# Kernel tuning notes

Hardware: AMD Instinct MI355X
Metric: run time of the kernel (lower is better)

## Reference

```python
import jax, jax.numpy as jnp
import numpy as np
import math

B, S, H = 8, 1024, 768
NH = 12
DH = H // NH


def _linear(x, W, b):
    # torch Linear: y = x @ W.T + b, W: [out, in]
    return jnp.einsum('bsd,ed->bse', x, W) + b


def _split_heads(x):
    # [B,S,H] -> [B,NH,S,DH]
    b, s, _ = x.shape
    return x.reshape(b, s, NH, DH).transpose(0, 2, 1, 3)


def _attend(q, k, v):
    # q,k,v: [B,NH,S,DH]
    scores = jnp.einsum('bhqd,bhkd->bhqk', q, k) / math.sqrt(DH)
    probs = jax.nn.softmax(scores, axis=-1)
    ctx = jnp.einsum('bhqk,bhkd->bhqd', probs, v)
    b, h, s, d = ctx.shape
    return ctx.transpose(0, 2, 1, 3).reshape(b, s, h * d)


def setup_inputs() -> dict:
    key = jax.random.key(0)
    ks = jax.random.split(key, 20)
    sc = 1.0 / math.sqrt(H)
    inp = {
        'hidden_statesx': jax.random.normal(ks[0], (B, S, H), jnp.float32),
        'hidden_statesy': jax.random.normal(ks[1], (B, S, H), jnp.float32),
    }
    names = ['Wq', 'Wk', 'Wv', 'Wo', 'Wqd', 'Wkd', 'Wvd', 'Wod']
    for i, n in enumerate(names):
        inp[n] = jax.random.normal(ks[2 + i], (H, H), jnp.float32) * sc
        inp['b' + n[1:]] = jnp.zeros((H,), jnp.float32)
    inp['w11'] = jnp.full((1,), 0.5, jnp.float32)
    inp['w12'] = jnp.full((1,), 0.5, jnp.float32)
    inp['w21'] = jnp.full((1,), 0.5, jnp.float32)
    inp['w22'] = jnp.full((1,), 0.5, jnp.float32)
    return inp


def reference(hidden_statesx, hidden_statesy,
              Wq, bq, Wk, bk, Wv, bv, Wo, bo,
              Wqd, bqd, Wkd, bkd, Wvd, bvd, Wod, bod,
              w11, w12, w21, w22):
    q = _split_heads(_linear(hidden_statesx, Wq, bq))
    k = _split_heads(_linear(hidden_statesx, Wk, bk))
    v = _split_heads(_linear(hidden_statesx, Wv, bv))
    qd = _split_heads(_linear(hidden_statesy, Wqd, bqd))
    kd = _split_heads(_linear(hidden_statesy, Wkd, bkd))
    vd = _split_heads(_linear(hidden_statesy, Wvd, bvd))

    # self-attention on x and y streams
    attention_sx = _linear(_attend(q, k, v), Wo, bo)
    attention_sy = _linear(_attend(qd, kd, vd), Wod, bod)
    # cross attentions (mba mode)
    attention_cx = _linear(_attend(q, kd, vd), Wo, bo)
    attention_cy = _linear(_attend(qd, k, v), Wod, bod)

    attention_sx = w11 * attention_sx + w12 * attention_cx
    attention_sy = w21 * attention_sy + w22 * attention_cy
    return attention_sx, attention_sy
```

## Files before the change

kernel.cpp:

```cpp
#include <hip/hip_runtime.h>

typedef __bf16 bf16;
typedef __bf16 bf16x8 __attribute__((ext_vector_type(8)));
typedef float f32x4 __attribute__((ext_vector_type(4)));

#define HD 768
#define ELTS 6291456
#define WELTS 589824

__device__ __forceinline__ void gld_lds16(const bf16* g, bf16* l) {
  __builtin_amdgcn_global_load_lds((const __attribute__((address_space(1))) void*)g,
                                   (__attribute__((address_space(3))) void*)l, 16, 0, 0);
}

__device__ __forceinline__ float rdscalar(const void* p, int f) {
  return f ? (float)((const bf16*)p)[0] : ((const float*)p)[0];
}

__device__ __forceinline__ float exp2fast(float x) {
#if __has_builtin(__builtin_amdgcn_exp2f)
  return __builtin_amdgcn_exp2f(x);
#else
  return __builtin_exp2f(x);
#endif
}

__global__ void probe_dtype(const unsigned int* __restrict__ x, int* flag) {
  const int t = threadIdx.x;
  int bad = 0;
#pragma unroll
  for (int i = 0; i < 4; ++i) {
    unsigned int wd = x[t * 4 + i];
    unsigned int e0 = (wd >> 7) & 0xFF;
    unsigned int e1 = (wd >> 23) & 0xFF;
    bad += (e0 >= 134) + (e1 >= 134);
  }
  unsigned long long m = __ballot(bad > 0);
  if (t == 0) *flag = (m == 0ULL) ? 1 : 0;
}

struct CvtArgs {
  const float* src[20];
  bf16* dst[20];
  int n[20];
  const int* flag;
};
__global__ __launch_bounds__(256) void convert_inputs(CvtArgs a) {
  if (*a.flag) return;
  const int seg = blockIdx.y;
  const float* s = a.src[seg];
  bf16* d = a.dst[seg];
  const int n4 = a.n[seg] >> 2;
  for (int i = blockIdx.x * blockDim.x + threadIdx.x; i < n4; i += gridDim.x * blockDim.x) {
    f32x4 v = *(const f32x4*)(s + i * 4);
    bf16 o[4];
#pragma unroll
    for (int e = 0; e < 4; ++e) o[e] = (bf16)v[e];
    *(unsigned long long*)(d + i * 4) = *(unsigned long long*)o;
  }
}

struct GemmArgs {
  const void* A[6];
  const void* Ac[6];
  const void* W[6];
  const void* Wc[6];
  const void* bias[6];
  const void* biasc[6];
  const void* s0[6];
  const void* s1[6];
  void* C[6];
  float cmul[6];
  int c_fixed[6];
  int vt[6];
  int ext_w[6];
  long long out_elem_off[6];
  const int* flag;
};

__global__ __launch_bounds__(256) void gemm_bt(GemmArgs args) {
  const int g = blockIdx.z;
  const int f = *args.flag;
  const bool c_bf = args.c_fixed[g] || f;
  const bool w_f32 = (!f) && args.ext_w[g];
  const bf16* __restrict__ A = (const bf16*)(f ? args.A[g] : args.Ac[g]);
  const void* __restrict__ Wp = f ? args.W[g] : args.Wc[g];
  const void* __restrict__ bias = f ? args.bias[g] : args.biasc[g];
  bf16* Cb = (bf16*)args.C[g] + args.out_elem_off[g];
  float* Cf = (float*)args.C[g] + args.out_elem_off[g];
  float bscale = 1.0f;
  if (args.s0[g]) bscale = rdscalar(args.s0[g], f) + rdscalar(args.s1[g], f);
  const float cmul = args.cmul[g];

  const int m0 = blockIdx.x * 128;
  const int n0 = blockIdx.y * 128;
  const int t = threadIdx.x;
  const int lane = t & 63;
  const int w = t >> 6;
  const int wm = (w >> 1) * 64, wn = (w & 1) * 64;

  __shared__ __attribute__((aligned(16))) bf16 As[128 * 64];
  __shared__ __attribute__((aligned(16))) bf16 Bs[128 * 64];

  f32x4 acc[4][4] = {};

  const int row_s = t >> 3, slot_s = t & 7;
  const int gswz = (slot_s ^ (row_s & 7)) << 3;

  const int fr = lane & 15;
  const int l4 = lane >> 4;
  const int sR0 = ((l4) ^ (fr & 7)) << 3;
  const int sR1 = ((4 + l4) ^ (fr & 7)) << 3;

  for (int kb = 0; kb < 12; ++kb) {
    const int k0 = kb * 64;
#pragma unroll
    for (int i = 0; i < 4; ++i) {
      const int row = row_s + i * 32;
      gld_lds16(A + (size_t)(m0 + row) * HD + k0 + gswz, As + (t + i * 256) * 8);
    }
    if (!w_f32) {
#pragma unroll
      for (int i = 0; i < 4; ++i) {
        const int row = row_s + i * 32;
        gld_lds16((const bf16*)Wp + (size_t)(n0 + row) * HD + k0 + gswz, Bs + (t + i * 256) * 8);
      }
    } else {
      const float* Wf = (const float*)Wp;
#pragma unroll
      for (int i = 0; i < 4; ++i) {
        const int row = row_s + i * 32;
        const size_t src = (size_t)(n0 + row) * HD + k0 + gswz;
        f32x4 u0 = *(const f32x4*)(Wf + src), u1 = *(const f32x4*)(Wf + src + 4);
        bf16x8 v;
#pragma unroll
        for (int e = 0; e < 4; ++e) { v[e] = (bf16)u0[e]; v[e + 4] = (bf16)u1[e]; }
        *(bf16x8*)(Bs + (t + i * 256) * 8) = v;
      }
    }
    __syncthreads();
#pragma unroll
    for (int kk = 0; kk < 2; ++kk) {
      const int sR = kk ? sR1 : sR0;
      bf16x8 af[4], bfr[4];
#pragma unroll
      for (int mi = 0; mi < 4; ++mi)
        af[mi] = *(const bf16x8*)(As + (wm + mi * 16 + fr) * 64 + sR);
#pragma unroll
      for (int ni = 0; ni < 4; ++ni)
        bfr[ni] = *(const bf16x8*)(Bs + (wn + ni * 16 + fr) * 64 + sR);
#pragma unroll
      for (int mi = 0; mi < 4; ++mi)
#pragma unroll
        for (int ni = 0; ni < 4; ++ni)
          acc[mi][ni] = __builtin_amdgcn_mfma_f32_16x16x32_bf16(af[mi], bfr[ni], acc[mi][ni], 0, 0, 0);
    }
    __syncthreads();
  }

  const int rq = (lane >> 4) * 4;
  const int is_vt = args.vt[g];
#pragma unroll
  for (int ni = 0; ni < 4; ++ni) {
    const int col = n0 + wn + ni * 16 + fr;
    const float bv = (w_f32 ? ((const float*)bias)[col]
                            : (float)((const bf16*)bias)[col]) * bscale;
#pragma unroll
    for (int mi = 0; mi < 4; ++mi) {
      const int row = m0 + wm + mi * 16 + rq;
      if (is_vt) {
        const int bb = row >> 10, s = row & 1023;
        const int hh = col >> 6, d = col & 63;
        bf16 tmp[4];
#pragma unroll
        for (int r = 0; r < 4; ++r) tmp[r] = (bf16)((acc[mi][ni][r] + bv) * cmul);
        *(unsigned long long*)(Cb + (((size_t)(bb * 12 + hh)) << 16) + (d << 10) + s) =
            *(const unsigned long long*)tmp;
      } else {
#pragma unroll
        for (int r = 0; r < 4; ++r) {
          const float val = (acc[mi][ni][r] + bv) * cmul;
          if (c_bf) Cb[(size_t)(row + r) * HD + col] = (bf16)val;
          else      Cf[(size_t)(row + r) * HD + col] = val;
        }
      }
    }
  }
}

__global__ __launch_bounds__(256, 4) void attn_mba(
    const bf16* __restrict__ Q, const bf16* __restrict__ Kx, const bf16* __restrict__ Vtx,
    const bf16* __restrict__ Qd, const bf16* __restrict__ Kd, const bf16* __restrict__ Vtd,
    const void* w11, const void* w12, const void* w21, const void* w22,
    bf16* ctxX, bf16* ctxY, const int* flag) {
  const int linear = blockIdx.x + (blockIdx.y << 4);
  const int swz = (linear & 7) * 192 + (linear >> 3);
  const int qb = swz & 15;
  const int bh = swz >> 4;
  const int b = bh / 12;
  const int f = *flag;

  const float wgtX[2] = {rdscalar(w11, f), rdscalar(w12, f)};
  const float wgtY[2] = {rdscalar(w22, f), rdscalar(w21, f)};

  const size_t tok0 = (size_t)b * 1024;
  const size_t vbase = (size_t)bh * 65536;
  const int fcol = (bh - b * 12) * 64;
  const int q0 = qb * 64;

  __shared__ __attribute__((aligned(16))) bf16 smem[16384];
  bf16* Ks = smem;
  bf16* Vs = smem + 8192;

  const int t = threadIdx.x, lane = t & 63, w = t >> 6;
  const int l15 = lane & 15, l4 = lane >> 4;

  auto stage = [&](int nit) {
    const bf16* Kc = nit < 16 ? Kx : Kd;
    const bf16* Vc = nit < 16 ? Vtx : Vtd;
    const int kt = nit & 15;
    bf16* Kb = Ks + (nit & 1) * 4096;
    bf16* Vb = Vs + (nit & 1) * 4096;
#pragma unroll
    for (int i = 0; i < 2; ++i) {
      const int q = t + i * 256;
      const int g = q >> 3, slot = q & 7;
      const int gs = (slot ^ (g & 7)) << 3;
      const int kp = (g & 32) + ((g & 12) << 1) + ((g & 16) >> 2) + (g & 3);
      gld_lds16(Kc + (tok0 + kt * 64 + kp) * HD + fcol + gs, Kb + q * 8);
      gld_lds16(Vc + vbase + (size_t)g * 1024 + kt * 64 + gs, Vb + q * 8);
    }
  };

  stage(0);

  const int qrow = w * 16 + l15;
  const bf16* qb0 = Q  + (tok0 + q0 + qrow) * HD + fcol;
  const bf16* qb1 = Qd + (tok0 + q0 + qrow) * HD + fcol;
  bf16x8 qf[2][2];
  qf[0][0] = *(const bf16x8*)(qb0 + (l4 << 3));
  qf[0][1] = *(const bf16x8*)(qb0 + ((4 + l4) << 3));
  qf[1][0] = *(const bf16x8*)(qb1 + (l4 << 3));
  qf[1][1] = *(const bf16x8*)(qb1 + ((4 + l4) << 3));

  int koff0[4], koff1[4];
#pragma unroll
  for (int mi = 0; mi < 4; ++mi) {
    const int kr = mi * 16 + l15;
    koff0[mi] = kr * 64 + ((l4 ^ (kr & 7)) << 3);
    koff1[mi] = kr * 64 + (((4 + l4) ^ (kr & 7)) << 3);
  }

  __syncthreads();

  f32x4 mixX[4] = {}, mixY[4] = {};
  f32x4 oacc[2][4] = {};
  float m_s[2] = {-INFINITY, -INFINITY};
  float l_s[2] = {0.0f, 0.0f};

  for (int it = 0; it < 32; ++it) {
    if (it) __syncthreads();
    if (it + 1 < 32) stage(it + 1);
    const bf16* Kb = Ks + (it & 1) * 4096;
    const bf16* Vb = Vs + (it & 1) * 4096;

#pragma unroll
    for (int s2 = 0; s2 < 2; ++s2) {
      float pv[4][4];
      float mx = -INFINITY;
      __builtin_amdgcn_s_setprio(1);
#pragma unroll
      for (int mi = 0; mi < 4; ++mi) {
        bf16x8 kf0 = *(const bf16x8*)(Kb + koff0[mi]);
        bf16x8 kf1 = *(const bf16x8*)(Kb + koff1[mi]);
        f32x4 s = {};
        s = __builtin_amdgcn_mfma_f32_16x16x32_bf16(kf0, qf[s2][0], s, 0, 0, 0);
        s = __builtin_amdgcn_mfma_f32_16x16x32_bf16(kf1, qf[s2][1], s, 0, 0, 0);
        pv[mi][0] = s[0]; pv[mi][1] = s[1]; pv[mi][2] = s[2]; pv[mi][3] = s[3];
        mx = fmaxf(fmaxf(mx, s[0]), s[1]);
        mx = fmaxf(fmaxf(mx, s[2]), s[3]);
      }
      __builtin_amdgcn_s_setprio(0);
      mx = fmaxf(mx, __shfl_xor(mx, 16));
      mx = fmaxf(mx, __shfl_xor(mx, 32));

      if (!__all(mx <= m_s[s2] + 8.0f)) {
        const float mnew = fmaxf(m_s[s2], mx);
        const float alpha = exp2fast(m_s[s2] - mnew);
        l_s[s2] *= alpha;
#pragma unroll
        for (int mi = 0; mi < 4; ++mi) oacc[s2][mi] *= alpha;
        m_s[s2] = mnew;
      }

      float sum = 0.0f;
#pragma unroll
      for (int mi = 0; mi < 4; ++mi)
#pragma unroll
        for (int r = 0; r < 4; ++r) {
          pv[mi][r] = exp2fast(pv[mi][r] - m_s[s2]);
          sum += pv[mi][r];
        }
      sum += __shfl_xor(sum, 16);
      sum += __shfl_xor(sum, 32);
      l_s[s2] += sum;

#pragma unroll
      for (int c = 0; c < 2; ++c) {
        bf16x8 pf;
#pragma unroll
        for (int j = 0; j < 8; ++j)
          pf[j] = (bf16)pv[2 * c + (j >> 2)][j & 3];
        __builtin_amdgcn_s_setprio(1);
#pragma unroll
        for (int mi = 0; mi < 4; ++mi) {
          bf16x8 vf = *(const bf16x8*)(Vb + (c ? koff1[mi] : koff0[mi]));
          oacc[s2][mi] = __builtin_amdgcn_mfma_f32_16x16x32_bf16(vf, pf, oacc[s2][mi], 0, 0, 0);
        }
        __builtin_amdgcn_s_setprio(0);
      }
    }

    if ((it & 15) == 15) {
      const int ph = it >> 4;
      const float scX = wgtX[ph] / l_s[0];
      const float scY = wgtY[ph] / l_s[1];
#pragma unroll
      for (int mi = 0; mi < 4; ++mi) {
#pragma unroll
        for (int r = 0; r < 4; ++r) {
          mixX[mi][r] += scX * oacc[0][mi][r];
          mixY[mi][r] += scY * oacc[1][mi][r];
        }
        oacc[0][mi] = f32x4{};
        oacc[1][mi] = f32x4{};
      }
      m_s[0] = m_s[1] = -INFINITY;
      l_s[0] = l_s[1] = 0.0f;
    }
  }

  __syncthreads();
  bf16* TX = smem;
  bf16* TY = smem + 4608;
#pragma unroll
  for (int mi = 0; mi < 4; ++mi)
#pragma unroll
    for (int r = 0; r < 4; ++r) {
      TX[qrow * 72 + mi * 16 + l4 * 4 + r] = (bf16)mixX[mi][r];
      TY[qrow * 72 + mi * 16 + l4 * 4 + r] = (bf16)mixY[mi][r];
    }
  __syncthreads();
#pragma unroll
  for (int i = 0; i < 2; ++i) {
    const int q = t + i * 256;
    const int g = q >> 3, dc = (q & 7) * 8;
    *(bf16x8*)(ctxX + (tok0 + q0 + g) * HD + fcol + dc) = *(const bf16x8*)(TX + g * 72 + dc);
    *(bf16x8*)(ctxY + (tok0 + q0 + g) * HD + fcol + dc) = *(const bf16x8*)(TY + g * 72 + dc);
  }
}

extern "C" void kernel_launch(void* const* d_in, const int* in_sizes, int n_in,
                              void* d_out, int out_size, void* d_ws, size_t ws_size,
                              hipStream_t stream) {
  (void)in_sizes; (void)n_in; (void)out_size;
  const void* x = d_in[0];
  const void* y = d_in[1];

  bf16* ws = (bf16*)d_ws;
  bf16* Qb   = ws + 0ull * ELTS;
  bf16* Kb   = ws + 1ull * ELTS;
  bf16* Vtb  = ws + 2ull * ELTS;
  bf16* Qdb  = ws + 3ull * ELTS;
  bf16* Kdb  = ws + 4ull * ELTS;
  bf16* Vtdb = ws + 5ull * ELTS;
  bf16* ctxX = Qb;
  bf16* ctxY = Qdb;
  int* flag = (int*)(ws + 6ull * ELTS);

  const size_t extra_elems = 6ull * ELTS + 32 + 2ull * WELTS + 2 * 768;
  const bool big_ws = ws_size >= extra_elems * sizeof(bf16);
  bf16* extraW = ws + 6ull * ELTS + 32;
  bf16* extraB = extraW + 2ull * WELTS;

  bf16* cb = (bf16*)d_out;
  bf16* xb = cb;
  bf16* yb = cb + (size_t)ELTS;
  bf16* Wcv = cb + 2ull * ELTS;
  bf16* bcv = Wcv + 6ull * WELTS;

  probe_dtype<<<dim3(1), dim3(64), 0, stream>>>((const unsigned int*)x, flag);

  CvtArgs ca;
  int nseg = 14;
  {
    const int wsrc[6] = {2, 4, 6, 10, 12, 14};
    ca.src[0] = (const float*)x;  ca.dst[0] = xb;  ca.n[0] = ELTS;
    ca.src[1] = (const float*)y;  ca.dst[1] = yb;  ca.n[1] = ELTS;
    for (int i = 0; i < 6; ++i) {
      ca.src[2 + i] = (const float*)d_in[wsrc[i]];
      ca.dst[2 + i] = Wcv + (size_t)i * WELTS;
      ca.n[2 + i] = WELTS;
      ca.src[8 + i] = (const float*)d_in[wsrc[i] + 1];
      ca.dst[8 + i] = bcv + (size_t)i * 768;
      ca.n[8 + i] = 768;
    }
    if (big_ws) {
      ca.src[14] = (const float*)d_in[8];  ca.dst[14] = extraW;         ca.n[14] = WELTS;
      ca.src[15] = (const float*)d_in[16]; ca.dst[15] = extraW + WELTS; ca.n[15] = WELTS;
      ca.src[16] = (const float*)d_in[9];  ca.dst[16] = extraB;         ca.n[16] = 768;
      ca.src[17] = (const float*)d_in[17]; ca.dst[17] = extraB + 768;   ca.n[17] = 768;
      nseg = 18;
    }
    ca.flag = flag;
  }
  convert_inputs<<<dim3(512, nseg), dim3(256), 0, stream>>>(ca);

  GemmArgs gq;
  {
    const void* A6[6]  = {x, x, x, y, y, y};
    const void* Ac6[6] = {xb, xb, xb, yb, yb, yb};
    const int di[6] = {2, 4, 6, 10, 12, 14};
    bf16* C6[6] = {Qb, Kb, Vtb, Qdb, Kdb, Vtdb};
    for (int i = 0; i < 6; ++i) {
      gq.A[i] = A6[i]; gq.Ac[i] = Ac6[i];
      gq.W[i] = d_in[di[i]]; gq.Wc[i] = Wcv + (size_t)i * WELTS;
      gq.bias[i] = d_in[di[i] + 1]; gq.biasc[i] = bcv + (size_t)i * 768;
      gq.s0[i] = nullptr; gq.s1[i] = nullptr; gq.C[i] = C6[i];
      gq.cmul[i] = (i == 0 || i == 3) ? 0.18033688011112042f : 1.0f;
      gq.c_fixed[i] = 1; gq.ext_w[i] = 0; gq.out_elem_off[i] = 0;
      gq.vt[i] = (i == 2 || i == 5) ? 1 : 0;
    }
    gq.flag = flag;
  }
  gemm_bt<<<dim3(64, 6, 6), dim3(256), 0, stream>>>(gq);

  attn_mba<<<dim3(16, 96), dim3(256), 0, stream>>>(
      Qb, Kb, Vtb, Qdb, Kdb, Vtdb, d_in[18], d_in[19], d_in[20], d_in[21],
      ctxX, ctxY, flag);

  GemmArgs gp;
  for (int i = 0; i < 6; ++i) {
    gp.A[i] = ctxX; gp.Ac[i] = ctxX;
    gp.W[i] = d_in[8]; gp.Wc[i] = d_in[8];
    gp.bias[i] = d_in[9]; gp.biasc[i] = d_in[9];
    gp.s0[i] = d_in[18]; gp.s1[i] = d_in[19]; gp.C[i] = d_out;
    gp.cmul[i] = 1.0f; gp.c_fixed[i] = 0; gp.vt[i] = 0;
    gp.ext_w[i] = 1; gp.out_elem_off[i] = 0;
  }
  gp.A[1] = ctxY; gp.Ac[1] = ctxY;
  gp.W[1] = d_in[16]; gp.Wc[1] = d_in[16];
  gp.bias[1] = d_in[17]; gp.biasc[1] = d_in[17];
  gp.s0[1] = d_in[20]; gp.s1[1] = d_in[21];
  gp.out_elem_off[1] = (long long)ELTS;
  if (big_ws) {
    gp.Wc[0] = extraW;         gp.biasc[0] = extraB;       gp.ext_w[0] = 0;
    gp.Wc[1] = extraW + WELTS; gp.biasc[1] = extraB + 768; gp.ext_w[1] = 0;
  }
  gp.flag = flag;
  gemm_bt<<<dim3(64, 6, 2), dim3(256), 0, stream>>>(gp);
}
```

Measured before the change: 415.1 us.

## Remap GEMM blocks per XCD and simplify attention address math

The GEMM kernel now maps its linear block index so that consecutive M-tiles of the same group/N-tile land on the same XCD, aiming to improve L2 reuse of weight tiles across chiplets. In the attention kernel, the staging offsets for K/V loads are hoisted out of the loop. Per-tile LDS offsets are derived from a single base using XOR instead of arrays. The max and sum reductions are vectorized with tree-shaped f32x4 operations to shorten dependency chains. These changes trade some setup complexity for fewer per-iteration integer ops and fewer live registers. The block remap assumes a specific grid shape (64 x 6 x groups).

```diff
diff --git a/kernel.cpp b/kernel.cpp
--- a/kernel.cpp
+++ b/kernel.cpp
@@ -23,6 +23,13 @@
 #else
   return __builtin_exp2f(x);
 #endif
+}
+
+__device__ __forceinline__ f32x4 vmax4(f32x4 a, f32x4 b) {
+  f32x4 r;
+#pragma unroll
+  for (int e = 0; e < 4; ++e) r[e] = fmaxf(a[e], b[e]);
+  return r;
 }
 
 __global__ void probe_dtype(const unsigned int* __restrict__ x, int* flag) {
@@ -79,7 +86,16 @@
 };
 
 __global__ __launch_bounds__(256) void gemm_bt(GemmArgs args) {
-  const int g = blockIdx.z;
+  const int linear = blockIdx.x + ((blockIdx.y + blockIdx.z * 6) << 6);
+  const int xcd = linear & 7;
+  const int pos = linear >> 3;
+  const int m0i = (xcd << 3) | (pos & 7);
+  const int nz = pos >> 3;
+  const int g = nz / 6;
+  const int n0i = nz - g * 6;
+  const int m0 = m0i * 128;
+  const int n0 = n0i * 128;
+
   const int f = *args.flag;
   const bool c_bf = args.c_fixed[g] || f;
   const bool w_f32 = (!f) && args.ext_w[g];
@@ -92,8 +108,6 @@
   if (args.s0[g]) bscale = rdscalar(args.s0[g], f) + rdscalar(args.s1[g], f);
   const float cmul = args.cmul[g];
 
-  const int m0 = blockIdx.x * 128;
-  const int n0 = blockIdx.y * 128;
   const int t = threadIdx.x;
   const int lane = t & 63;
   const int w = t >> 6;
@@ -215,41 +229,40 @@
   const int t = threadIdx.x, lane = t & 63, w = t >> 6;
   const int l15 = lane & 15, l4 = lane >> 4;
 
+  const int g0 = t >> 3, slot0 = t & 7;
+  const int g1 = g0 + 32;
+  const int gs = (slot0 ^ (g0 & 7)) << 3;
+  const int kp0 = (g0 & 32) + ((g0 & 12) << 1) + ((g0 & 16) >> 2) + (g0 & 3);
+  const int kp1 = (g1 & 32) + ((g1 & 12) << 1) + ((g1 & 16) >> 2) + (g1 & 3);
+  const size_t koffg0 = (tok0 + kp0) * HD + fcol + gs;
+  const size_t koffg1 = (tok0 + kp1) * HD + fcol + gs;
+  const size_t voffg0 = vbase + (size_t)g0 * 1024 + gs;
+  const size_t voffg1 = vbase + (size_t)g1 * 1024 + gs;
+
   auto stage = [&](int nit) {
     const bf16* Kc = nit < 16 ? Kx : Kd;
     const bf16* Vc = nit < 16 ? Vtx : Vtd;
-    const int kt = nit & 15;
+    const int kt64 = (nit & 15) * 64;
     bf16* Kb = Ks + (nit & 1) * 4096;
     bf16* Vb = Vs + (nit & 1) * 4096;
-#pragma unroll
-    for (int i = 0; i < 2; ++i) {
-      const int q = t + i * 256;
-      const int g = q >> 3, slot = q & 7;
-      const int gs = (slot ^ (g & 7)) << 3;
-      const int kp = (g & 32) + ((g & 12) << 1) + ((g & 16) >> 2) + (g & 3);
-      gld_lds16(Kc + (tok0 + kt * 64 + kp) * HD + fcol + gs, Kb + q * 8);
-      gld_lds16(Vc + vbase + (size_t)g * 1024 + kt * 64 + gs, Vb + q * 8);
-    }
+    gld_lds16(Kc + koffg0 + (size_t)kt64 * HD, Kb + t * 8);
+    gld_lds16(Kc + koffg1 + (size_t)kt64 * HD, Kb + (t + 256) * 8);
+    gld_lds16(Vc + voffg0 + kt64, Vb + t * 8);
+    gld_lds16(Vc + voffg1 + kt64, Vb + (t + 256) * 8);
   };
 
   stage(0);
 
   const int qrow = w * 16 + l15;
-  const bf16* qb0 = Q  + (tok0 + q0 + qrow) * HD + fcol;
-  const bf16* qb1 = Qd + (tok0 + q0 + qrow) * HD + fcol;
+  const bf16* qp0 = Q  + (tok0 + q0 + qrow) * HD + fcol;
+  const bf16* qp1 = Qd + (tok0 + q0 + qrow) * HD + fcol;
   bf16x8 qf[2][2];
-  qf[0][0] = *(const bf16x8*)(qb0 + (l4 << 3));
-  qf[0][1] = *(const bf16x8*)(qb0 + ((4 + l4) << 3));
-  qf[1][0] = *(const bf16x8*)(qb1 + (l4 << 3));
-  qf[1][1] = *(const bf16x8*)(qb1 + ((4 + l4) << 3));
-
-  int koff0[4], koff1[4];
-#pragma unroll
-  for (int mi = 0; mi < 4; ++mi) {
-    const int kr = mi * 16 + l15;
-    koff0[mi] = kr * 64 + ((l4 ^ (kr & 7)) << 3);
-    koff1[mi] = kr * 64 + (((4 + l4) ^ (kr & 7)) << 3);
-  }
+  qf[0][0] = *(const bf16x8*)(qp0 + (l4 << 3));
+  qf[0][1] = *(const bf16x8*)(qp0 + ((4 + l4) << 3));
+  qf[1][0] = *(const bf16x8*)(qp1 + (l4 << 3));
+  qf[1][1] = *(const bf16x8*)(qp1 + ((4 + l4) << 3));
+
+  const int kbase = l15 * 64 + ((l4 ^ (l15 & 7)) << 3);
 
   __syncthreads();
 
@@ -266,21 +279,20 @@
 
 #pragma unroll
     for (int s2 = 0; s2 < 2; ++s2) {
-      float pv[4][4];
-      float mx = -INFINITY;
+      f32x4 sv[4];
       __builtin_amdgcn_s_setprio(1);
 #pragma unroll
       for (int mi = 0; mi < 4; ++mi) {
-        bf16x8 kf0 = *(const bf16x8*)(Kb + koff0[mi]);
-        bf16x8 kf1 = *(const bf16x8*)(Kb + koff1[mi]);
+        bf16x8 kf0 = *(const bf16x8*)(Kb + (kbase + mi * 1024));
+        bf16x8 kf1 = *(const bf16x8*)(Kb + ((kbase + mi * 1024) ^ 32));
         f32x4 s = {};
         s = __builtin_amdgcn_mfma_f32_16x16x32_bf16(kf0, qf[s2][0], s, 0, 0, 0);
         s = __builtin_amdgcn_mfma_f32_16x16x32_bf16(kf1, qf[s2][1], s, 0, 0, 0);
-        pv[mi][0] = s[0]; pv[mi][1] = s[1]; pv[mi][2] = s[2]; pv[mi][3] = s[3];
-        mx = fmaxf(fmaxf(mx, s[0]), s[1]);
-        mx = fmaxf(fmaxf(mx, s[2]), s[3]);
+        sv[mi] = s;
       }
       __builtin_amdgcn_s_setprio(0);
+      f32x4 mq = vmax4(vmax4(sv[0], sv[1]), vmax4(sv[2], sv[3]));
+      float mx = fmaxf(fmaxf(mq[0], mq[1]), fmaxf(mq[2], mq[3]));
       mx = fmaxf(mx, __shfl_xor(mx, 16));
       mx = fmaxf(mx, __shfl_xor(mx, 32));
 
@@ -293,14 +305,17 @@
         m_s[s2] = mnew;
       }
 
-      float sum = 0.0f;
-#pragma unroll
-      for (int mi = 0; mi < 4; ++mi)
-#pragma unroll
-        for (int r = 0; r < 4; ++r) {
-          pv[mi][r] = exp2fast(pv[mi][r] - m_s[s2]);
-          sum += pv[mi][r];
-        }
+      const float mreg = m_s[s2];
+      f32x4 sum4 = {};
+#pragma unroll
+      for (int mi = 0; mi < 4; ++mi) {
+        f32x4 e;
+#pragma unroll
+        for (int r = 0; r < 4; ++r) e[r] = exp2fast(sv[mi][r] - mreg);
+        sv[mi] = e;
+        sum4 += e;
+      }
+      float sum = (sum4[0] + sum4[1]) + (sum4[2] + sum4[3]);
       sum += __shfl_xor(sum, 16);
       sum += __shfl_xor(sum, 32);
       l_s[s2] += sum;
@@ -310,11 +325,11 @@
         bf16x8 pf;
 #pragma unroll
         for (int j = 0; j < 8; ++j)
-          pf[j] = (bf16)pv[2 * c + (j >> 2)][j & 3];
+          pf[j] = (bf16)sv[2 * c + (j >> 2)][j & 3];
         __builtin_amdgcn_s_setprio(1);
 #pragma unroll
         for (int mi = 0; mi < 4; ++mi) {
-          bf16x8 vf = *(const bf16x8*)(Vb + (c ? koff1[mi] : koff0[mi]));
+          bf16x8 vf = *(const bf16x8*)(Vb + ((kbase + mi * 1024) ^ (c << 5)));
           oacc[s2][mi] = __builtin_amdgcn_mfma_f32_16x16x32_bf16(vf, pf, oacc[s2][mi], 0, 0, 0);
         }
         __builtin_amdgcn_s_setprio(0);
```

After: 420.5 us. Within noise of the previous version (+1.3%).
